# Performance work log

Hardware: AMD Instinct MI355X
Metric: run time of the kernel (lower is better)

## Reference

```python
import jax, jax.numpy as jnp
import numpy as np

K = 5  # top-k margin
B, C = 4096, 50257

def setup_inputs() -> dict:
    key = jax.random.key(0)
    kx, ky = jax.random.split(key)
    x = jax.random.normal(kx, (B, C), dtype=jnp.float32)
    y = jax.random.randint(ky, (B,), 0, C, dtype=jnp.int64)
    return {"x": x, "y": y}

def reference(x, y):
    b = x.shape[0]
    # scatter 0 at the true-class position (mask out s_y from the top-k pool)
    x_no_y = x.at[jnp.arange(b), y].set(0.0)
    # top-k (same as full descending sort + slice, but O(C) selection)
    s_topk, _ = jax.lax.top_k(x_no_y, K)          # [B, K]
    s_y = jnp.take_along_axis(x, y[:, None], -1)   # [B, 1]
    m = jnp.mean(s_topk, axis=-1)                  # [B]
    # faithful to torch: [B] - [B,1] broadcasts to [B,B] before the mean
    return jnp.mean(jnp.maximum(1.0 + m - s_y, 0.0))
```

## Files before the change

kernel.cpp:

```cpp
#include <hip/hip_runtime.h>
#include <cfloat>

#define BDIM 256
constexpr int BB = 4096;
constexpr int CC = 50257;

typedef float f32x4 __attribute__((ext_vector_type(4)));

__global__ __launch_bounds__(BDIM) void topk_kernel(const float* __restrict__ x,
                                                    const int* __restrict__ y,
                                                    float* __restrict__ m_out,
                                                    float* __restrict__ sy_out) {
    const int row = blockIdx.x;
    const int tid = threadIdx.x;
    const float* __restrict__ xr = x + (size_t)row * CC;
    const int target = y[row];

    __shared__ float sy_sh;
    __shared__ float tl[BDIM][5];

    float a0 = -FLT_MAX, a1 = -FLT_MAX, a2 = -FLT_MAX, a3 = -FLT_MAX, a4 = -FLT_MAX;
    float b0 = -FLT_MAX, b1 = -FLT_MAX, b2 = -FLT_MAX, b3 = -FLT_MAX, b4 = -FLT_MAX;

#define INSA(val)                                                       \
    do {                                                                \
        float _v = (val);                                               \
        if (_v > a4) {                                                  \
            a4 = _v;                                                    \
            if (a4 > a3) { float _w = a3; a3 = a4; a4 = _w; }           \
            if (a3 > a2) { float _w = a2; a2 = a3; a3 = _w; }           \
            if (a2 > a1) { float _w = a1; a1 = a2; a2 = _w; }           \
            if (a1 > a0) { float _w = a0; a0 = a1; a1 = _w; }           \
        }                                                               \
    } while (0)

#define INSB(val)                                                       \
    do {                                                                \
        float _v = (val);                                               \
        if (_v > b4) {                                                  \
            b4 = _v;                                                    \
            if (b4 > b3) { float _w = b3; b3 = b4; b4 = _w; }           \
            if (b3 > b2) { float _w = b2; b2 = b3; b3 = _w; }           \
            if (b2 > b1) { float _w = b1; b1 = b2; b2 = _w; }           \
            if (b1 > b0) { float _w = b0; b0 = b1; b1 = _w; }           \
        }                                                               \
    } while (0)

#define MASK4(vec, j0)                                                  \
    do {                                                                \
        int _d = target - (j0);                                         \
        if ((unsigned)_d < 4u) {                                        \
            sy_sh = (vec)[_d];                                          \
            (vec)[_d] = 0.0f;                                           \
        }                                                               \
    } while (0)

#define PROC(jidx, raw)                                                 \
    do {                                                                \
        float _r = (raw);                                               \
        float _c = _r;                                                  \
        if ((jidx) == target) { sy_sh = _r; _c = 0.0f; }                \
        INSA(_c);                                                       \
    } while (0)

    const int align = (4 - (row & 3)) & 3;

    if (tid < align) {
        PROC(tid, xr[tid]);
    }

    const int nvec = (CC - align) >> 2;
    const f32x4* __restrict__ xv = reinterpret_cast<const f32x4*>(xr + align);

    int i = tid;
    for (; i + BDIM < nvec; i += 2 * BDIM) {
        f32x4 v0 = __builtin_nontemporal_load(&xv[i]);
        f32x4 v1 = __builtin_nontemporal_load(&xv[i + BDIM]);
        const int j0 = align + (i << 2);
        const int j1 = align + ((i + BDIM) << 2);
        MASK4(v0, j0);
        MASK4(v1, j1);
        INSA(v0[0]); INSB(v0[1]); INSA(v0[2]); INSB(v0[3]);
        INSA(v1[0]); INSB(v1[1]); INSA(v1[2]); INSB(v1[3]);
    }
    for (; i < nvec; i += BDIM) {
        f32x4 v0 = __builtin_nontemporal_load(&xv[i]);
        const int j0 = align + (i << 2);
        MASK4(v0, j0);
        INSA(v0[0]); INSB(v0[1]); INSA(v0[2]); INSB(v0[3]);
    }

    for (int j = align + (nvec << 2) + tid; j < CC; j += BDIM) {
        PROC(j, xr[j]);
    }

    INSA(b0); INSA(b1); INSA(b2); INSA(b3); INSA(b4);

    tl[tid][0] = a0; tl[tid][1] = a1; tl[tid][2] = a2; tl[tid][3] = a3; tl[tid][4] = a4;
    __syncthreads();

    for (int s = BDIM / 2; s >= 1; s >>= 1) {
        if (tid < s) {
            float o0 = tl[tid + s][0], o1 = tl[tid + s][1], o2 = tl[tid + s][2],
                  o3 = tl[tid + s][3], o4 = tl[tid + s][4];
            INSA(o0); INSA(o1); INSA(o2); INSA(o3); INSA(o4);
            tl[tid][0] = a0; tl[tid][1] = a1; tl[tid][2] = a2; tl[tid][3] = a3; tl[tid][4] = a4;
        }
        __syncthreads();
    }

    if (tid == 0) {
        m_out[row]  = (a0 + a1 + a2 + a3 + a4) * 0.2f;
        sy_out[row] = sy_sh;
    }
#undef PROC
#undef MASK4
#undef INSA
#undef INSB
}

__global__ __launch_bounds__(BDIM) void pair_kernel(const float* __restrict__ m,
                                                    const float* __restrict__ sy,
                                                    float* __restrict__ partial) {
    const int i = blockIdx.x;
    const int tid = threadIdx.x;
    const float syi = sy[i];
    float acc = 0.0f;
    for (int j = tid; j < BB; j += BDIM) {
        acc += fmaxf(1.0f + m[j] - syi, 0.0f);
    }
    __shared__ float red[BDIM];
    red[tid] = acc;
    __syncthreads();
    for (int s = BDIM / 2; s >= 1; s >>= 1) {
        if (tid < s) red[tid] += red[tid + s];
        __syncthreads();
    }
    if (tid == 0) partial[i] = red[0];
}

__global__ __launch_bounds__(BDIM) void final_kernel(const float* __restrict__ partial,
                                                     float* __restrict__ out) {
    const int tid = threadIdx.x;
    float acc = 0.0f;
    for (int j = tid; j < BB; j += BDIM) acc += partial[j];
    __shared__ float red[BDIM];
    red[tid] = acc;
    __syncthreads();
    for (int s = BDIM / 2; s >= 1; s >>= 1) {
        if (tid < s) red[tid] += red[tid + s];
        __syncthreads();
    }
    if (tid == 0) out[0] = red[0] / 16777216.0f;
}

extern "C" void kernel_launch(void* const* d_in, const int* in_sizes, int n_in,
                              void* d_out, int out_size, void* d_ws, size_t ws_size,
                              hipStream_t stream) {
    const float* x = (const float*)d_in[0];
    const int*   y = (const int*)d_in[1];
    float* out = (float*)d_out;

    float* m       = (float*)d_ws;
    float* sy      = m + BB;
    float* partial = sy + BB;

    topk_kernel<<<BB, BDIM, 0, stream>>>(x, y, m, sy);
    pair_kernel<<<BB, BDIM, 0, stream>>>(m, sy, partial);
    final_kernel<<<1, BDIM, 0, stream>>>(partial, out);
}
```

Measured before the change: 154.8 us.

## Split each row's top-k scan across two blocks and merge partial top-5s

Each row is now handled by two blocks, each scanning half the vectorized columns. Each block writes its local top-5 to workspace, and a new merge kernel combines the two sorted lists into the row mean. The main loop is also unrolled to four vector loads per iteration. The aim is more blocks in flight and more memory-level parallelism on a bandwidth-bound scan, at the cost of an extra kernel launch and workspace traffic.

```diff
diff --git a/kernel.cpp b/kernel.cpp
--- a/kernel.cpp
+++ b/kernel.cpp
@@ -7,12 +7,14 @@
 
 typedef float f32x4 __attribute__((ext_vector_type(4)));
 
-__global__ __launch_bounds__(BDIM) void topk_kernel(const float* __restrict__ x,
-                                                    const int* __restrict__ y,
-                                                    float* __restrict__ m_out,
-                                                    float* __restrict__ sy_out) {
-    const int row = blockIdx.x;
-    const int tid = threadIdx.x;
+__global__ __launch_bounds__(BDIM) void topk_half_kernel(const float* __restrict__ x,
+                                                         const int* __restrict__ y,
+                                                         float* __restrict__ t5_ws,
+                                                         float* __restrict__ sy_out) {
+    const int bid  = blockIdx.x;
+    const int row  = bid >> 1;
+    const int half = bid & 1;
+    const int tid  = threadIdx.x;
     const float* __restrict__ xr = x + (size_t)row * CC;
     const int target = y[row];
 
@@ -64,34 +66,40 @@
     } while (0)
 
     const int align = (4 - (row & 3)) & 3;
-
-    if (tid < align) {
-        PROC(tid, xr[tid]);
-    }
-
-    const int nvec = (CC - align) >> 2;
+    const int nvec  = (CC - align) >> 2;
+    const int halfv = nvec >> 1;
+    const int vbeg  = half ? halfv : 0;
+    const int vend  = half ? nvec  : halfv;
+
+    if (!half) {
+        if (tid < align) PROC(tid, xr[tid]);
+    } else {
+        for (int j = align + (nvec << 2) + tid; j < CC; j += BDIM) PROC(j, xr[j]);
+    }
+
     const f32x4* __restrict__ xv = reinterpret_cast<const f32x4*>(xr + align);
 
-    int i = tid;
-    for (; i + BDIM < nvec; i += 2 * BDIM) {
+    int i = vbeg + tid;
+    for (; i + 3 * BDIM < vend; i += 4 * BDIM) {
         f32x4 v0 = __builtin_nontemporal_load(&xv[i]);
         f32x4 v1 = __builtin_nontemporal_load(&xv[i + BDIM]);
+        f32x4 v2 = __builtin_nontemporal_load(&xv[i + 2 * BDIM]);
+        f32x4 v3 = __builtin_nontemporal_load(&xv[i + 3 * BDIM]);
         const int j0 = align + (i << 2);
         const int j1 = align + ((i + BDIM) << 2);
-        MASK4(v0, j0);
-        MASK4(v1, j1);
+        const int j2 = align + ((i + 2 * BDIM) << 2);
+        const int j3 = align + ((i + 3 * BDIM) << 2);
+        MASK4(v0, j0); MASK4(v1, j1); MASK4(v2, j2); MASK4(v3, j3);
         INSA(v0[0]); INSB(v0[1]); INSA(v0[2]); INSB(v0[3]);
         INSA(v1[0]); INSB(v1[1]); INSA(v1[2]); INSB(v1[3]);
-    }
-    for (; i < nvec; i += BDIM) {
+        INSA(v2[0]); INSB(v2[1]); INSA(v2[2]); INSB(v2[3]);
+        INSA(v3[0]); INSB(v3[1]); INSA(v3[2]); INSB(v3[3]);
+    }
+    for (; i < vend; i += BDIM) {
         f32x4 v0 = __builtin_nontemporal_load(&xv[i]);
         const int j0 = align + (i << 2);
         MASK4(v0, j0);
         INSA(v0[0]); INSB(v0[1]); INSA(v0[2]); INSB(v0[3]);
-    }
-
-    for (int j = align + (nvec << 2) + tid; j < CC; j += BDIM) {
-        PROC(j, xr[j]);
     }
 
     INSA(b0); INSA(b1); INSA(b2); INSA(b3); INSA(b4);
@@ -110,13 +118,34 @@
     }
 
     if (tid == 0) {
-        m_out[row]  = (a0 + a1 + a2 + a3 + a4) * 0.2f;
-        sy_out[row] = sy_sh;
+        float* t5 = t5_ws + (size_t)bid * 5;
+        t5[0] = a0; t5[1] = a1; t5[2] = a2; t5[3] = a3; t5[4] = a4;
+        const int lo = half ? align + (halfv << 2) : 0;
+        const int hi = half ? CC : align + (halfv << 2);
+        if (target >= lo && target < hi) sy_out[row] = sy_sh;
     }
 #undef PROC
 #undef MASK4
 #undef INSA
 #undef INSB
+}
+
+__global__ __launch_bounds__(BDIM) void merge_kernel(const float* __restrict__ t5_ws,
+                                                     float* __restrict__ m_out) {
+    const int r = blockIdx.x * BDIM + threadIdx.x;
+    if (r >= BB) return;
+    const float* __restrict__ p = t5_ws + (size_t)r * 10;
+    const float* A = p;
+    const float* B = p + 5;
+    float s = 0.0f;
+    int ia = 0, ib = 0;
+    #pragma unroll
+    for (int k = 0; k < 5; ++k) {
+        float av = A[ia], bv = B[ib];
+        if (av >= bv) { s += av; ++ia; }
+        else          { s += bv; ++ib; }
+    }
+    m_out[r] = s * 0.2f;
 }
 
 __global__ __launch_bounds__(BDIM) void pair_kernel(const float* __restrict__ m,
@@ -161,11 +190,13 @@
     const int*   y = (const int*)d_in[1];
     float* out = (float*)d_out;
 
-    float* m       = (float*)d_ws;
-    float* sy      = m + BB;
-    float* partial = sy + BB;
-
-    topk_kernel<<<BB, BDIM, 0, stream>>>(x, y, m, sy);
+    float* t5      = (float*)d_ws;
+    float* sy      = t5 + 2 * BB * 5;
+    float* m       = sy + BB;
+    float* partial = m + BB;
+
+    topk_half_kernel<<<2 * BB, BDIM, 0, stream>>>(x, y, t5, sy);
+    merge_kernel<<<BB / BDIM, BDIM, 0, stream>>>(t5, m);
     pair_kernel<<<BB, BDIM, 0, stream>>>(m, sy, partial);
     final_kernel<<<1, BDIM, 0, stream>>>(partial, out);
 }
```

After: 152.5 us (median of 2 runs). No clear change (-1.5%).
